# Performance work log

Measured on AMD Instinct MI355X. Metric: run time of the kernel, lower is better.

Reference implementation:

```python
import jax, jax.numpy as jnp
import numpy as np
import math

B, L, H = 32, 2048, 8
DMET, SDIM = 16, 27
DM, NL, DS, TE = 256, 4, 64, 256
LT = L + H - 1
DT_MIN, DT_MAX = 1e-3, 0.1


def setup_inputs() -> dict:
    key = jax.random.key(0)
    ks = jax.random.split(key, 24)
    inp = {
        'x_past': jax.random.normal(ks[0], (B, L, DMET), jnp.float32),
        'noisy_future': jax.random.normal(ks[1], (B, H, 1), jnp.float32),
        't': jax.random.uniform(ks[2], (B,), jnp.float32),
        'x_future': jax.random.normal(ks[3], (B, H - 1, DMET), jnp.float32),
        'static_attr': jax.random.normal(ks[4], (B, 1, SDIM), jnp.float32),
        # MPFourier buffers
        'freqs': 2 * math.pi * jax.random.normal(ks[5], (TE,), jnp.float32),
        'phases': 2 * math.pi * jax.random.uniform(ks[6], (TE,), jnp.float32),
        # input projection (d_met+1+static_dim -> d_model)
        'in_W': jax.random.normal(ks[7], (DMET + 1 + SDIM, DM), jnp.float32) / np.sqrt(DMET + 1 + SDIM),
        'in_b': jnp.zeros((DM,), jnp.float32),
        # time MLP
        'tm_W1': jax.random.normal(ks[8], (TE, 2 * TE), jnp.float32) / np.sqrt(TE),
        'tm_b1': jnp.zeros((2 * TE,), jnp.float32),
        'tm_W2': jax.random.normal(ks[9], (2 * TE, DM), jnp.float32) / np.sqrt(2 * TE),
        'tm_b2': jnp.zeros((DM,), jnp.float32),
        # stacked S4D (LTI) block params, leading dim = n_layers
        'log_dt': jax.random.uniform(ks[10], (NL, DM), jnp.float32) * (math.log(DT_MAX) - math.log(DT_MIN)) + math.log(DT_MIN),
        'A_re': -0.5 * jnp.ones((NL, DM, DS), jnp.float32),
        'A_im': math.pi * jnp.broadcast_to(jnp.arange(DS, dtype=jnp.float32), (NL, DM, DS)),
        'C_re': jax.random.normal(ks[11], (NL, DM, DS), jnp.float32) * (0.5 ** 0.5),
        'C_im': jax.random.normal(ks[12], (NL, DM, DS), jnp.float32) * (0.5 ** 0.5),
        'D': jax.random.normal(ks[13], (NL, DM), jnp.float32),
        'out_W': jax.random.normal(ks[14], (NL, DM, 2 * DM), jnp.float32) / np.sqrt(DM),
        'out_b': jnp.zeros((NL, 2 * DM), jnp.float32),
        # batchnorm
        'bn_gamma': jnp.ones((NL, DM), jnp.float32),
        'bn_beta': jnp.zeros((NL, DM), jnp.float32),
        # head
        'head_W1': jax.random.normal(ks[15], (DM, DM // 2), jnp.float32) / np.sqrt(DM),
        'head_b1': jnp.zeros((DM // 2,), jnp.float32),
        'head_W2': jax.random.normal(ks[16], (DM // 2, 1), jnp.float32) / np.sqrt(DM // 2),
        'head_b2': jnp.zeros((1,), jnp.float32),
    }
    return inp


def _ssm_block(u, log_dt, A_re, A_im, C_re, C_im, D, out_W, out_b):
    # u: [B, d, Lc]. S4D-style diagonal SSM via FFT causal convolution.
    Lc = u.shape[-1]
    dt = jnp.exp(log_dt)                                 # [d]
    A = A_re + 1j * A_im                                 # [d, n], Re(A) < 0
    dtA = dt[:, None] * A                                # [d, n]
    Ck = (C_re + 1j * C_im) * jnp.expm1(dtA) / A         # ZOH-style discretized C
    van = jnp.exp(dtA[:, :, None] * jnp.arange(Lc))      # [d, n, Lc] Vandermonde
    K = 2.0 * jnp.einsum('dn,dnl->dl', Ck, van).real     # [d, Lc]
    nfft = 2 * Lc
    y = jnp.fft.irfft(jnp.fft.rfft(u, nfft) * jnp.fft.rfft(K, nfft)[None], nfft)[..., :Lc]
    y = jax.nn.gelu(y + D[None, :, None] * u)
    z = jnp.einsum('bdl,de->bel', y, out_W) + out_b[None, :, None]  # [B, 2d, Lc]
    z1, z2 = jnp.split(z, 2, axis=1)
    return z1 * jax.nn.sigmoid(z2)                       # GLU


def _batchnorm1d(h, gamma, beta):
    # h: [B, d, Lc]; training-mode batch statistics, eps matches torch default.
    mean = h.mean(axis=(0, 2), keepdims=True)
    var = ((h - mean) ** 2).mean(axis=(0, 2), keepdims=True)
    return (h - mean) * jax.lax.rsqrt(var + 1e-5) * gamma[None, :, None] + beta[None, :, None]


def reference(x_past, noisy_future, t, x_future, static_attr,
              freqs, phases, in_W, in_b, tm_W1, tm_b1, tm_W2, tm_b2,
              log_dt, A_re, A_im, C_re, C_im, D, out_W, out_b,
              bn_gamma, bn_beta, head_W1, head_b1, head_W2, head_b2):
    Bc = x_past.shape[0]
    # MPFourier time features
    t_feats = jnp.cos(t[:, None] * freqs[None, :] + phases[None, :]) * math.sqrt(2)
    t_b = jax.nn.silu(t_feats @ tm_W1 + tm_b1) @ tm_W2 + tm_b2     # [B, DM]
    # feature fusion
    all_met = jnp.concatenate([x_past, x_future], axis=1)          # [B, LT, DMET]
    all_flow = jnp.concatenate([jnp.zeros((Bc, L - 1, 1), x_past.dtype), noisy_future], axis=1)
    static_seq = jnp.broadcast_to(static_attr[:, :1, :], (Bc, LT, SDIM))
    feats = jnp.concatenate([all_met, all_flow, static_seq], axis=-1)
    h = feats @ in_W + in_b                                        # [B, LT, DM]
    h = h.at[:, L - 1:, :].add(t_b[:, None, :])                    # time_full conditioning
    h = jnp.transpose(h, (0, 2, 1))                                # [B, DM, LT]
    for i in range(NL):
        z = _ssm_block(h, log_dt[i], A_re[i], A_im[i], C_re[i], C_im[i],
                       D[i], out_W[i], out_b[i])
        h = _batchnorm1d(h + z, bn_gamma[i], bn_beta[i])           # dropout = identity (eval)
    h = jnp.transpose(h, (0, 2, 1))                                # [B, LT, DM]
    out = jax.nn.silu(h @ head_W1 + head_b1) @ head_W2 + head_b2   # [B, LT, 1]
    return out[:, -H:, :]
```

## Files before the change

kernel.cpp:

```cpp
#include <hip/hip_runtime.h>
#include <hip/hip_bf16.h>
#include <math.h>

#define B_   32
#define L_   2048
#define H_   8
#define DMET 16
#define SDIM 27
#define DM   256
#define NL   4
#define DS   64
#define TE   256
#define LT   2055
#define LTR  2176
#define TCH  128
#define NC   17
#define COLS 544
#define NTOT (B_ * LT)

typedef __attribute__((ext_vector_type(8))) short short8;
typedef __attribute__((ext_vector_type(4))) short short4v;
typedef __attribute__((ext_vector_type(4))) float floatx4;

__device__ __forceinline__ float sigmoidf_(float x) {
    float e = __builtin_amdgcn_exp2f(-1.4426950408889634f * x);
    return __builtin_amdgcn_rcpf(1.0f + e);
}

__device__ __forceinline__ float gelu_tanh(float x) {
    float inner = 1.5957691216057308f * fmaf(0.044715f * x * x, x, x);
    return x * sigmoidf_(inner);
}

__device__ __forceinline__ float fexp_(float x) {
    return __builtin_amdgcn_exp2f(1.4426950408889634f * x);
}
__device__ __forceinline__ float fsin_(float ph) {
    float r = ph * 0.15915494309189535f;
    r = r - floorf(r);
    return __builtin_amdgcn_sinf(r);
}
__device__ __forceinline__ float fcos_(float ph) {
    float r = ph * 0.15915494309189535f;
    r = r - floorf(r);
    return __builtin_amdgcn_cosf(r);
}

__device__ __forceinline__ short bfs(float x) {
    __hip_bfloat16 h = __float2bfloat16(x);
    return *(short*)&h;
}

__device__ __forceinline__ float sbf(short s) {
    unsigned u = ((unsigned)(unsigned short)s) << 16;
    return __uint_as_float(u);
}

__device__ __forceinline__ void glds16(const void* g, void* l) {
    __builtin_amdgcn_global_load_lds(
        (const __attribute__((address_space(1))) unsigned*)g,
        (__attribute__((address_space(3))) unsigned*)l, 16, 0, 0);
}

#define BARV(n) do {                                                          \
    asm volatile("s_waitcnt vmcnt(" #n ") lgkmcnt(0)" ::: "memory");          \
    __builtin_amdgcn_s_barrier();                                             \
    asm volatile("" ::: "memory");                                            \
} while (0)

__global__ __launch_bounds__(256) void time_mlp_kernel(
    const float* __restrict__ t, const float* __restrict__ freqs,
    const float* __restrict__ phases,
    const float* __restrict__ W1, const float* __restrict__ b1,
    const float* __restrict__ W2, const float* __restrict__ b2,
    float* __restrict__ tb) {
    int b = blockIdx.x;
    int tid = threadIdx.x;
    __shared__ float f[TE];
    __shared__ float hid[2 * TE];
    float tv = t[b];
    f[tid] = cosf(fmaf(tv, freqs[tid], phases[tid])) * 1.4142135623730951f;
    __syncthreads();
    float a0 = b1[tid], a1 = b1[tid + TE];
    for (int k = 0; k < TE; ++k) {
        float fk = f[k];
        a0 = fmaf(fk, W1[k * 2 * TE + tid], a0);
        a1 = fmaf(fk, W1[k * 2 * TE + tid + TE], a1);
    }
    hid[tid]      = a0 * sigmoidf_(a0);
    hid[tid + TE] = a1 * sigmoidf_(a1);
    __syncthreads();
    float acc = b2[tid];
    for (int j = 0; j < 2 * TE; ++j)
        acc = fmaf(hid[j], W2[j * DM + tid], acc);
    tb[b * DM + tid] = acc;
}

__global__ __launch_bounds__(256) void wt_prep_kernel(
    const float* __restrict__ out_W, __hip_bfloat16* __restrict__ Wtp) {
    int bid = blockIdx.x;
    int layer = bid >> 8, k = bid & 255;
    int e = threadIdx.x;
    const float* src = out_W + ((size_t)layer * 256 + k) * 512;
    #pragma unroll
    for (int q = 0; q < 2; ++q) {
        int ee = e + q * 256;
        int P = ee & 255, half = ee >> 8;
        int by = P >> 6, pp = P & 63;
        int g = pp >> 5;
        int tcol = (pp & 31) + half * 32;
        int c = by * 128 + g * 64 + tcol;
        Wtp[((size_t)layer * 512 + c) * 256 + k] = __float2bfloat16(src[ee]);
    }
}

__global__ __launch_bounds__(256) void input_proj_kernel(
    const float* __restrict__ xp, const float* __restrict__ nf,
    const float* __restrict__ xf, const float* __restrict__ sa,
    const float* __restrict__ inW, const float* __restrict__ inb,
    const float* __restrict__ tb, __hip_bfloat16* __restrict__ Ub) {
    int b  = blockIdx.y;
    int l0 = blockIdx.x * 256;
    int tx = threadIdx.x;
    int l  = l0 + tx;

    __shared__ float feats[256][18];
    __shared__ float Ws[17][DM];
    __shared__ float sdot[DM];
    __shared__ float tbs[DM];
    __shared__ float sstat[SDIM];

    if (tx < SDIM) sstat[tx] = sa[b * SDIM + tx];
    for (int k = 0; k < 17; ++k) Ws[k][tx] = inW[k * DM + tx];
    tbs[tx] = tb[b * DM + tx];

    bool valid = (l < LT);
    if (valid) {
        const float* src = (l < L_) ? &xp[((size_t)b * L_ + l) * DMET]
                                    : &xf[((size_t)b * (H_ - 1) + (l - L_)) * DMET];
        #pragma unroll
        for (int k = 0; k < DMET; ++k) feats[tx][k] = src[k];
        feats[tx][16] = (l >= L_ - 1) ? nf[b * H_ + (l - (L_ - 1))] : 0.0f;
    }
    __syncthreads();

    float sd = 0.0f;
    for (int k = 0; k < SDIM; ++k)
        sd = fmaf(sstat[k], inW[(17 + k) * DM + tx], sd);
    sdot[tx] = sd;
    __syncthreads();

    if (l >= LTR) return;
    size_t baseb = ((size_t)b * DM) * LTR + l;
    if (!valid) {
        __hip_bfloat16 z = __float2bfloat16(0.0f);
        for (int d = 0; d < DM; ++d) Ub[baseb + (size_t)d * LTR] = z;
        return;
    }
    bool cond = (l >= L_ - 1);
    for (int d = 0; d < DM; ++d) {
        float acc = inb[d] + sdot[d] + (cond ? tbs[d] : 0.0f);
        #pragma unroll
        for (int k = 0; k < 17; ++k)
            acc = fmaf(feats[tx][k], Ws[k][d], acc);
        Ub[baseb + (size_t)d * LTR] = __float2bfloat16(acc);
    }
}

__global__ __launch_bounds__(256) void prep_kernel(
    const float* __restrict__ log_dt,
    const float* __restrict__ A_re, const float* __restrict__ A_im,
    const float* __restrict__ C_re, const float* __restrict__ C_im,
    const float* __restrict__ Dp,
    const float* __restrict__ gamma, const float* __restrict__ beta,
    float* __restrict__ stats, float* __restrict__ scsh,
    __hip_bfloat16* __restrict__ Abig, __hip_bfloat16* __restrict__ SA,
    float* __restrict__ Rsh, float* __restrict__ T1sh, int layer) {
    int d = blockIdx.x;
    int t = threadIdx.x;
    __shared__ float sAr[64], sAi[64], sCkr[64], sCki[64];
    __shared__ float kap[TCH];
    __shared__ float csum[TCH];
    __shared__ float s_sc, s_sh;

    if (t == 0) {
        float sc, sh;
        if (layer == 0) { sc = 1.0f; sh = 0.0f; }
        else {
            float s = stats[d], q = stats[DM + d];
            float mean = s * (1.0f / NTOT);
            float var  = q * (1.0f / NTOT) - mean * mean;
            sc = rsqrtf(var + 1e-5f) * gamma[(layer - 1) * DM + d];
            sh = beta[(layer - 1) * DM + d] - mean * sc;
        }
        s_sc = sc; s_sh = sh;
        scsh[d] = sc; scsh[DM + d] = sh;
        stats[d] = 0.0f; stats[DM + d] = 0.0f;
    }
    __syncthreads();
    float sc = s_sc, sh = s_sh;

    float dt = expf(log_dt[layer * DM + d]);
    float Dd = Dp[layer * DM + d];
    if (t < 64) {
        size_t ab = ((size_t)layer * DM + d) * DS + t;
        float Ar = A_re[ab], Ai = A_im[ab], Cr = C_re[ab], Ci = C_im[ab];
        float ar = dt * Ar, ai = dt * Ai;
        float e = expf(ar);
        float wre = e * cosf(ai), wim = e * sinf(ai);
        float mr = wre - 1.0f, mi = wim;
        float den = 1.0f / (Ar * Ar + Ai * Ai);
        float qr = (mr * Ar + mi * Ai) * den, qi = (mi * Ar - mr * Ai) * den;
        sCkr[t] = Cr * qr - Ci * qi;
        sCki[t] = Cr * qi + Ci * qr;
        sAr[t] = ar;
        sAi[t] = ai;
        float s2 = sinf(0.5f * ai);
        float dr = fmaf(expm1f(ar), cosf(ai), -2.0f * s2 * s2);
        float di = e * sinf(ai);
        float a128 = 128.0f * ar, b128 = 128.0f * ai;
        float s2b = sinf(0.5f * b128);
        float nr = fmaf(expm1f(a128), cosf(b128), -2.0f * s2b * s2b);
        float ni = expf(a128) * sinf(b128);
        float dd2 = 1.0f / (dr * dr + di * di);
        float gr = (nr * dr + ni * di) * dd2;
        float gi = (ni * dr - nr * di) * dd2;
        Rsh[(size_t)d * 128 + t]      = sh * gr;
        Rsh[(size_t)d * 128 + 64 + t] = sh * gi;
    }
    __syncthreads();

    {
        int delta = t >> 1, half = t & 1;
        float fd = (float)delta;
        float p = 0.0f;
        #pragma unroll 8
        for (int n = half * 32; n < half * 32 + 32; ++n) {
            float er = fexp_(fd * sAr[n]);
            float ph = fd * sAi[n];
            p += er * (sCkr[n] * fcos_(ph) - sCki[n] * fsin_(ph));
        }
        p += __shfl_xor(p, 1);
        if (half == 0) kap[delta] = 2.0f * p + (delta == 0 ? Dd : 0.0f);
    }
    __syncthreads();

    if (t < 128) csum[t] = kap[t];
    __syncthreads();
    for (int off = 1; off < 128; off <<= 1) {
        float v = 0.0f;
        if (t >= off && t < 128) v = csum[t - off];
        __syncthreads();
        if (t < 128) csum[t] += v;
        __syncthreads();
    }
    if (t < 128) T1sh[(size_t)d * 128 + t] = sh * csum[t];

    __hip_bfloat16* Ad = Abig + (size_t)d * TCH * 256;
    for (int idx = t; idx < TCH * TCH; idx += 256) {
        int i = idx >> 7, m = idx & 127;
        Ad[(size_t)i * 256 + m] = __float2bfloat16(m <= i ? sc * kap[i - m] : 0.0f);
    }
    for (int idx = t; idx < TCH * 64; idx += 256) {
        int i = idx >> 6, n = idx & 63;
        float fp = (float)(i + 1);
        float er = fexp_(fp * sAr[n]);
        float ph = fp * sAi[n];
        float c = fcos_(ph), s = fsin_(ph);
        float vr = er * (sCkr[n] * c - sCki[n] * s);
        float vi = er * (sCkr[n] * s + sCki[n] * c);
        Ad[(size_t)i * 256 + 128 + n] = __float2bfloat16(2.0f * vr);
        Ad[(size_t)i * 256 + 192 + n] = __float2bfloat16(-2.0f * vi);
    }
    __hip_bfloat16* Sd = SA + (size_t)d * TCH * TCH;
    for (int idx = t; idx < 64 * TCH; idx += 256) {
        int n = idx >> 7, m = idx & 127;
        float fp = (float)(127 - m);
        float er = sc * fexp_(fp * sAr[n]);
        float ph = fp * sAi[n];
        Sd[(size_t)n * 128 + m]        = __float2bfloat16(er * fcos_(ph));
        Sd[(size_t)(64 + n) * 128 + m] = __float2bfloat16(er * fsin_(ph));
    }
}

__global__ __launch_bounds__(256) void sgemm_kernel(
    const __hip_bfloat16* __restrict__ Ub, const __hip_bfloat16* __restrict__ SA,
    const float* __restrict__ Rsh, __hip_bfloat16* __restrict__ S) {
    int id = blockIdx.x;
    int xcd = id & 7, j = id >> 3;
    int dj = (j * 21846) >> 16;
    int d = xcd * 32 + dj;
    int g = j - dj * 3;
    int tid = threadIdx.x, wave = tid >> 6, lane = tid & 63;
    int lm = lane & 15, quad = lane >> 4;
    const __hip_bfloat16* SAd = SA + (size_t)d * TCH * TCH;

    __shared__ short Bs[12288];

    short8 a0r[4], a1r[4];
    #pragma unroll
    for (int kk = 0; kk < 4; ++kk) {
        a0r[kk] = *(const short8*)(SAd + (size_t)(wave * 32 + lm) * TCH + kk * 32 + quad * 8);
        a1r[kk] = *(const short8*)(SAd + (size_t)(wave * 32 + 16 + lm) * TCH + kk * 32 + quad * 8);
    }

    int ntS = (tid >> 6) & 3, qS = (tid >> 4) & 3, ccS = tid & 15;
    const __hip_bfloat16* srcB[3];
    #pragma unroll
    for (int t = 0; t < 3; ++t) {
        int col = (3 * g + t) * 64 + ntS * 16 + ccS;
        int colc = col < COLS ? col : COLS - 1;
        int bh = (colc * 241) >> 12;
        int c = colc - bh * 17;
        srcB[t] = Ub + ((size_t)bh * DM + d) * LTR + (size_t)c * TCH + qS * 8;
    }

    float4 rs0 = *(const float4*)(Rsh + (size_t)d * 128 + wave * 32 + quad * 4);
    float4 rs1 = *(const float4*)(Rsh + (size_t)d * 128 + wave * 32 + 16 + quad * 4);

    floatx4 acc[2][4];
    floatx4 zf = {0.f, 0.f, 0.f, 0.f};
    #pragma unroll
    for (int mi = 0; mi < 2; ++mi)
        #pragma unroll
        for (int nt = 0; nt < 4; ++nt) acc[mi][nt] = zf;

#define SG_STAGE(t_, kk0_, off_)                                              \
    {                                                                         \
        glds16(srcB[t_] + (kk0_) * 32,     (char*)Bs + (off_) + tid * 16);    \
        glds16(srcB[t_] + (kk0_ + 1) * 32, (char*)Bs + (off_) + 4096 + tid * 16); \
    }
#define SG_COMP(off_, kkA_)                                                   \
    {                                                                         \
        const short* bb_ = (const short*)((const char*)Bs + (off_));          \
        _Pragma("unroll")                                                     \
        for (int kk_ = 0; kk_ < 2; ++kk_) {                                   \
            _Pragma("unroll")                                                 \
            for (int nt_ = 0; nt_ < 4; ++nt_) {                               \
                short8 bv = *(const short8*)(bb_ + kk_ * 2048 + nt_ * 512 + lane * 8); \
                acc[0][nt_] = __builtin_amdgcn_mfma_f32_16x16x32_bf16(        \
                    a0r[(kkA_) + kk_], bv, acc[0][nt_], 0, 0, 0);             \
                acc[1][nt_] = __builtin_amdgcn_mfma_f32_16x16x32_bf16(        \
                    a1r[(kkA_) + kk_], bv, acc[1][nt_], 0, 0, 0);             \
            }                                                                 \
        }                                                                     \
    }
#define SG_EPI(cb_)                                                           \
    _Pragma("unroll")                                                         \
    for (int mi = 0; mi < 2; ++mi) {                                          \
        int row = wave * 32 + mi * 16 + quad * 4;                             \
        float4 rs = mi ? rs1 : rs0;                                           \
        _Pragma("unroll")                                                     \
        for (int nt_ = 0; nt_ < 4; ++nt_) {                                   \
            int col = (cb_) * 64 + nt_ * 16 + lm;                             \
            if (col < COLS) {                                                 \
                short4v o;                                                    \
                o[0] = bfs(acc[mi][nt_][0] + rs.x);                           \
                o[1] = bfs(acc[mi][nt_][1] + rs.y);                           \
                o[2] = bfs(acc[mi][nt_][2] + rs.z);                           \
                o[3] = bfs(acc[mi][nt_][3] + rs.w);                           \
                *(short4v*)(S + ((size_t)d * COLS + col) * TCH + row) = o;    \
            }                                                                 \
            acc[mi][nt_] = zf;                                                \
        }                                                                     \
    }

    SG_STAGE(0, 0, 0);
    SG_STAGE(0, 2, 8192);
    SG_STAGE(1, 0, 16384);
    BARV(4);
    SG_COMP(0, 0);
    BARV(2);
    SG_STAGE(1, 2, 0);
    SG_COMP(8192, 2);
    BARV(2);
    SG_STAGE(2, 0, 8192);
    SG_EPI(3 * g + 0);
    BARV(4);
    SG_COMP(16384, 0);
    BARV(2);
    SG_STAGE(2, 2, 16384);
    SG_COMP(0, 2);
    SG_EPI(3 * g + 1);
    BARV(2);
    SG_COMP(8192, 0);
    BARV(0);
    SG_COMP(16384, 2);
    SG_EPI(3 * g + 2);

#undef SG_STAGE
#undef SG_COMP
#undef SG_EPI
}

__global__ __launch_bounds__(64) void carry_kernel(
    __hip_bfloat16* __restrict__ SX,
    const float* __restrict__ log_dt,
    const float* __restrict__ A_re, const float* __restrict__ A_im,
    int layer) {
    int d = blockIdx.x, b = blockIdx.y;
    int n = threadIdx.x;
    float dt = expf(log_dt[layer * DM + d]);
    size_t ab = ((size_t)layer * DM + d) * DS + n;
    float Ar = A_re[ab], Ai = A_im[ab];
    float e = expf(dt * Ar);
    float wre = e * cosf(dt * Ai), wim = e * sinf(dt * Ai);
    #pragma unroll
    for (int t = 0; t < 7; ++t) {
        float r = wre * wre - wim * wim;
        wim = 2.0f * wre * wim; wre = r;
    }
    size_t base = ((size_t)d * COLS + (size_t)b * NC) * TCH + n;
    float sre[NC], sim[NC];
    #pragma unroll
    for (int c = 0; c < NC; ++c) {
        sre[c] = __bfloat162float(SX[base + (size_t)c * TCH]);
        sim[c] = __bfloat162float(SX[base + (size_t)c * TCH + 64]);
    }
    float xr = 0.0f, xi = 0.0f;
    #pragma unroll
    for (int c = 0; c < NC; ++c) {
        SX[base + (size_t)c * TCH]      = __float2bfloat16(xr);
        SX[base + (size_t)c * TCH + 64] = __float2bfloat16(xi);
        float nr = wre * xr - wim * xi + sre[c];
        xi = wre * xi + wim * xr + sim[c];
        xr = nr;
    }
}

__global__ __launch_bounds__(256) void mainscan_kernel(
    const __hip_bfloat16* __restrict__ Ub, const __hip_bfloat16* __restrict__ X,
    const __hip_bfloat16* __restrict__ Abig, const float* __restrict__ T1sh,
    __hip_bfloat16* __restrict__ Ybt) {
    int id = blockIdx.x;
    int xcd = id & 7, j = id >> 3;
    int dj = (j * 21846) >> 16;
    int d = xcd * 32 + dj;
    int g = j - dj * 3;
    int tid = threadIdx.x, wave = tid >> 6, lane = tid & 63;
    int lm = lane & 15, quad = lane >> 4;
    const __hip_bfloat16* Ad = Abig + (size_t)d * TCH * 256;

    __shared__ short Bs[24576];

    short8 a0r[8], a1r[8];
    #pragma unroll
    for (int kk = 0; kk < 8; ++kk) {
        a0r[kk] = *(const short8*)(Ad + (size_t)(wave * 32 + lm) * 256 + kk * 32 + quad * 8);
        a1r[kk] = *(const short8*)(Ad + (size_t)(wave * 32 + 16 + lm) * 256 + kk * 32 + quad * 8);
    }

    int ntS = (tid >> 6) & 3, qS = (tid >> 4) & 3, ccS = tid & 15;
    const __hip_bfloat16* srcU[3];
    const __hip_bfloat16* srcX[3];
    #pragma unroll
    for (int t = 0; t < 3; ++t) {
        int col = (3 * g + t) * 64 + ntS * 16 + ccS;
        int colc = col < COLS ? col : COLS - 1;
        int bh = (colc * 241) >> 12;
        int c = colc - bh * 17;
        srcU[t] = Ub + ((size_t)bh * DM + d) * LTR + (size_t)c * TCH + qS * 8;
        srcX[t] = X + ((size_t)d * COLS + colc) * TCH + qS * 8;
    }

    float4 t1a = *(const float4*)(T1sh + (size_t)d * 128 + wave * 32 + quad * 4);
    float4 t1b = *(const float4*)(T1sh + (size_t)d * 128 + wave * 32 + 16 + quad * 4);

    floatx4 acc[2][4];
    floatx4 zf = {0.f, 0.f, 0.f, 0.f};
    #pragma unroll
    for (int mi = 0; mi < 2; ++mi)
        #pragma unroll
        for (int nt = 0; nt < 4; ++nt) acc[mi][nt] = zf;

#define MS_STAGE_LO(t_, off_)                                                 \
    {                                                                         \
        _Pragma("unroll")                                                     \
        for (int k_ = 0; k_ < 4; ++k_)                                        \
            glds16(srcU[t_] + k_ * 32,                                        \
                   (char*)Bs + (off_) + k_ * 4096 + tid * 16);                \
    }
#define MS_STAGE_HI(t_, off_)                                                 \
    {                                                                         \
        _Pragma("unroll")                                                     \
        for (int k_ = 0; k_ < 4; ++k_)                                        \
            glds16(srcX[t_] + k_ * 32,                                        \
                   (char*)Bs + (off_) + k_ * 4096 + tid * 16);                \
    }
#define MS_COMP(off_, kkA_)                                                   \
    {                                                                         \
        const short* bb_ = (const short*)((const char*)Bs + (off_));          \
        _Pragma("unroll")                                                     \
        for (int kk_ = 0; kk_ < 4; ++kk_) {                                   \
            _Pragma("unroll")                                                 \
            for (int nt_ = 0; nt_ < 4; ++nt_) {                               \
                short8 bv = *(const short8*)(bb_ + kk_ * 2048 + nt_ * 512 + lane * 8); \
                acc[0][nt_] = __builtin_amdgcn_mfma_f32_16x16x32_bf16(        \
                    a0r[(kkA_) + kk_], bv, acc[0][nt_], 0, 0, 0);             \
                acc[1][nt_] = __builtin_amdgcn_mfma_f32_16x16x32_bf16(        \
                    a1r[(kkA_) + kk_], bv, acc[1][nt_], 0, 0, 0);             \
            }                                                                 \
        }                                                                     \
    }
#define MS_EPI(cb_)                                                           \
    _Pragma("unroll")                                                         \
    for (int mi = 0; mi < 2; ++mi) {                                          \
        int row0 = wave * 32 + mi * 16 + quad * 4;                            \
        float4 t1 = mi ? t1b : t1a;                                           \
        _Pragma("unroll")                                                     \
        for (int nt_ = 0; nt_ < 4; ++nt_) {                                   \
            int col = (cb_) * 64 + nt_ * 16 + lm;                             \
            if (col < COLS) {                                                 \
                int bh = (col * 241) >> 12;                                   \
                int c = col - bh * 17;                                        \
                int l0 = c * TCH + row0;                                      \
                float g0 = gelu_tanh(acc[mi][nt_][0] + t1.x);                 \
                float g1 = gelu_tanh(acc[mi][nt_][1] + t1.y);                 \
                float g2 = gelu_tanh(acc[mi][nt_][2] + t1.z);                 \
                float g3 = gelu_tanh(acc[mi][nt_][3] + t1.w);                 \
                __hip_bfloat16* dst = Ybt + ((size_t)bh * DM + d) * LTR + l0; \
                if (l0 + 3 < LT) {                                            \
                    short4v o;                                                \
                    o[0] = bfs(g0); o[1] = bfs(g1);                           \
                    o[2] = bfs(g2); o[3] = bfs(g3);                           \
                    *(short4v*)dst = o;                                       \
                } else {                                                      \
                    if (l0 + 0 < LT) dst[0] = __float2bfloat16(g0);           \
                    if (l0 + 1 < LT) dst[1] = __float2bfloat16(g1);           \
                    if (l0 + 2 < LT) dst[2] = __float2bfloat16(g2);           \
                    if (l0 + 3 < LT) dst[3] = __float2bfloat16(g3);           \
                }                                                             \
            }                                                                 \
            acc[mi][nt_] = zf;                                                \
        }                                                                     \
    }

    MS_STAGE_LO(0, 0);
    MS_STAGE_HI(0, 16384);
    MS_STAGE_LO(1, 32768);
    BARV(8);
    MS_COMP(0, 0);
    BARV(4);
    MS_STAGE_HI(1, 0);
    MS_COMP(16384, 4);
    BARV(4);
    MS_STAGE_LO(2, 16384);
    MS_EPI(3 * g + 0);
    BARV(8);
    MS_COMP(32768, 0);
    BARV(4);
    MS_STAGE_HI(2, 32768);
    MS_COMP(0, 4);
    MS_EPI(3 * g + 1);
    BARV(4);
    MS_COMP(16384, 0);
    BARV(0);
    MS_COMP(32768, 4);
    MS_EPI(3 * g + 2);

#undef MS_STAGE_LO
#undef MS_STAGE_HI
#undef MS_COMP
#undef MS_EPI
}

__global__ __launch_bounds__(256) void gemm_glu_mfma_kernel(
    const __hip_bfloat16* __restrict__ Ybt, __hip_bfloat16* __restrict__ Ub,
    const __hip_bfloat16* __restrict__ Wtp, const float* __restrict__ out_b,
    const float* __restrict__ scsh, float* __restrict__ stats, int layer) {
    int id = blockIdx.x;
    int r8 = id & 7, j = id >> 3;
    int by = r8 >> 1;
    int sub = (r8 & 1) * 272 + j;
    int bq = (sub * 3856) >> 16;
    int bx = sub - bq * 17;
    int b = bq;
    int tid = threadIdx.x;
    int wave = tid >> 6, lane = tid & 63;
    int lm = lane & 15, quad = lane >> 4;
    int l0 = bx * 128;

    __shared__ short lds[16384];

    const __hip_bfloat16* Wl = Wtp + (size_t)layer * 512 * 256 + (size_t)by * 128 * 256;

    int kp = tid >> 4;
    int l8 = tid & 15;
    const __hip_bfloat16* srcA = Ybt + ((size_t)b * DM + 2 * kp) * LTR + l0 + l8 * 8;
    int woff[8];
    {
        int qA = kp >> 2;
        #pragma unroll
        for (int jj = 0; jj < 8; ++jj) {
            int lloc = l8 * 8 + jj;
            int s4 = (qA + lloc + l8) & 3;
            woff[jj] = lloc * 32 + s4 * 8 + (kp & 3) * 2;
        }
    }
    int rB_[2], qB_[2];
    #pragma unroll
    for (int i = 0; i < 2; ++i) {
        int u = i * 256 + tid;
        int r = u >> 2;
        rB_[i] = r;
        qB_[i] = ((u & 3) - r - (r >> 3)) & 3;
    }
    int aoff[4], boff[4];
    #pragma unroll
    for (int mi = 0; mi < 4; ++mi) {
        int r = (wave >> 1) * 64 + mi * 16 + lm;
        aoff[mi] = r * 32 + ((quad + r + (r >> 3)) & 3) * 8;
    }
    #pragma unroll
    for (int ni = 0; ni < 4; ++ni) {
        int r = (wave & 1) * 64 + ni * 16 + lm;
        boff[ni] = r * 32 + ((quad + r + (r >> 3)) & 3) * 8;
    }

    floatx4 acc[4][4];
    floatx4 zf = {0.f, 0.f, 0.f, 0.f};
    #pragma unroll
    for (int mi = 0; mi < 4; ++mi)
        #pragma unroll
        for (int ni = 0; ni < 4; ++ni) acc[mi][ni] = zf;

#define STAGE_B(S, P)                                                         \
    {                                                                         \
        char* bb_ = (char*)(lds + (P) * 8192 + 4096);                         \
        _Pragma("unroll")                                                     \
        for (int i_ = 0; i_ < 2; ++i_)                                        \
            glds16(Wl + (size_t)rB_[i_] * 256 + (S) * 32 + qB_[i_] * 8,       \
                   bb_ + (i_ * 256 + tid) * 16);                              \
    }
#define LOAD_A(S, G0, G1)                                                     \
    {                                                                         \
        const __hip_bfloat16* pa_ = srcA + (size_t)(S) * 32 * LTR;            \
        G0 = *(const short8*)pa_;                                             \
        G1 = *(const short8*)(pa_ + LTR);                                     \
    }
#define WRITE_A(P, G0, G1)                                                    \
    {                                                                         \
        short* ab_ = lds + (P) * 8192;                                        \
        _Pragma("unroll")                                                     \
        for (int j_ = 0; j_ < 8; ++j_) {                                      \
            unsigned pk_ = (unsigned)(unsigned short)G0[j_] |                 \
                           ((unsigned)(unsigned short)G1[j_] << 16);          \
            *(unsigned*)(ab_ + woff[j_]) = pk_;                               \
        }                                                                     \
    }
#define COMPUTE(P)                                                            \
    {                                                                         \
        const short* ab_ = lds + (P) * 8192;                                  \
        const short* bb_ = ab_ + 4096;                                        \
        short8 af_[4], bf_[4];                                                \
        _Pragma("unroll")                                                     \
        for (int mi_ = 0; mi_ < 4; ++mi_)                                     \
            af_[mi_] = *(const short8*)(ab_ + aoff[mi_]);                     \
        _Pragma("unroll")                                                     \
        for (int ni_ = 0; ni_ < 4; ++ni_)                                     \
            bf_[ni_] = *(const short8*)(bb_ + boff[ni_]);                     \
        _Pragma("unroll")                                                     \
        for (int mi_ = 0; mi_ < 4; ++mi_)                                     \
            _Pragma("unroll")                                                 \
            for (int ni_ = 0; ni_ < 4; ++ni_)                                 \
                acc[mi_][ni_] = __builtin_amdgcn_mfma_f32_16x16x32_bf16(      \
                    af_[mi_], bf_[ni_], acc[mi_][ni_], 0, 0, 0);              \
    }
#define FENCE2                                                                \
    asm volatile("s_waitcnt vmcnt(2)" ::: "memory");                          \
    asm volatile("s_waitcnt lgkmcnt(0)" ::: "memory");                        \
    __builtin_amdgcn_sched_barrier(0);                                        \
    __builtin_amdgcn_s_barrier();
#define FENCE0                                                                \
    asm volatile("s_waitcnt vmcnt(0)" ::: "memory");                          \
    asm volatile("s_waitcnt lgkmcnt(0)" ::: "memory");                        \
    __builtin_amdgcn_sched_barrier(0);                                        \
    __builtin_amdgcn_s_barrier();

    short8 gE0, gE1, gO0, gO1;
    STAGE_B(0, 0);
    LOAD_A(0, gE0, gE1);
    WRITE_A(0, gE0, gE1);
    LOAD_A(1, gO0, gO1);
    asm volatile("s_waitcnt lgkmcnt(0)" ::: "memory");
    __builtin_amdgcn_sched_barrier(0);
    __builtin_amdgcn_s_barrier();

    STAGE_B(1, 1); COMPUTE(0); WRITE_A(1, gO0, gO1); LOAD_A(2, gE0, gE1); FENCE2;
    STAGE_B(2, 0); COMPUTE(1); WRITE_A(0, gE0, gE1); LOAD_A(3, gO0, gO1); FENCE2;
    STAGE_B(3, 1); COMPUTE(0); WRITE_A(1, gO0, gO1); LOAD_A(4, gE0, gE1); FENCE2;
    STAGE_B(4, 0); COMPUTE(1); WRITE_A(0, gE0, gE1); LOAD_A(5, gO0, gO1); FENCE2;
    STAGE_B(5, 1); COMPUTE(0); WRITE_A(1, gO0, gO1); LOAD_A(6, gE0, gE1); FENCE2;
    STAGE_B(6, 0); COMPUTE(1); WRITE_A(0, gE0, gE1); LOAD_A(7, gO0, gO1); FENCE2;
    STAGE_B(7, 1); COMPUTE(0); WRITE_A(1, gO0, gO1); FENCE0;
    COMPUTE(1);

#undef STAGE_B
#undef LOAD_A
#undef WRITE_A
#undef COMPUTE
#undef FENCE2
#undef FENCE0

    const float* bl = out_b + layer * 512;
    int Pbase = by * 64 + (wave & 1) * 32;
    int lw = l0 + (wave >> 1) * 64;
    #pragma unroll
    for (int ni = 0; ni < 2; ++ni) {
        int P = Pbase + ni * 16 + lm;
        float bz1 = bl[P], bz2 = bl[256 + P];
        float scP = scsh[P], shP = scsh[DM + P];
        __hip_bfloat16* ubrow = Ub + ((size_t)b * DM + P) * LTR;
        float sp = 0.f, sq = 0.f;
        #pragma unroll
        for (int mi = 0; mi < 4; ++mi) {
            int l0q = lw + mi * 16 + quad * 4;
            if (l0q >= LT) continue;
            floatx4 z1 = acc[mi][ni];
            floatx4 z2 = acc[mi][ni + 2];
            if (l0q + 4 <= LT) {
                short4v uv = *(const short4v*)(ubrow + l0q);
                float h0 = fmaf(scP, sbf(uv[0]), shP) + (z1[0] + bz1) * sigmoidf_(z2[0] + bz2);
                float h1 = fmaf(scP, sbf(uv[1]), shP) + (z1[1] + bz1) * sigmoidf_(z2[1] + bz2);
                float h2 = fmaf(scP, sbf(uv[2]), shP) + (z1[2] + bz1) * sigmoidf_(z2[2] + bz2);
                float h3 = fmaf(scP, sbf(uv[3]), shP) + (z1[3] + bz1) * sigmoidf_(z2[3] + bz2);
                short4v ov;
                ov[0] = bfs(h0); ov[1] = bfs(h1); ov[2] = bfs(h2); ov[3] = bfs(h3);
                *(short4v*)(ubrow + l0q) = ov;
                sp += (h0 + h1) + (h2 + h3);
                sq += (h0 * h0 + h1 * h1) + (h2 * h2 + h3 * h3);
            } else {
                #pragma unroll
                for (int r = 0; r < 4; ++r) {
                    int l = l0q + r;
                    if (l < LT) {
                        float uvv = __bfloat162float(ubrow[l]);
                        float hh = fmaf(scP, uvv, shP) + (z1[r] + bz1) * sigmoidf_(z2[r] + bz2);
                        ubrow[l] = __float2bfloat16(hh);
                        sp += hh; sq += hh * hh;
                    }
                }
            }
        }
        sp += __shfl_xor(sp, 16); sp += __shfl_xor(sp, 32);
        sq += __shfl_xor(sq, 16); sq += __shfl_xor(sq, 32);
        if (quad == 0) {
            atomicAdd(&stats[P], sp);
            atomicAdd(&stats[DM + P], sq);
        }
    }
}

__global__ __launch_bounds__(256) void statsfin_kernel(
    const float* __restrict__ stats,
    const float* __restrict__ gamma, const float* __restrict__ beta,
    float* __restrict__ scsh, int layer) {
    int d = threadIdx.x;
    float s = stats[d], q = stats[DM + d];
    float mean = s * (1.0f / NTOT);
    float var  = q * (1.0f / NTOT) - mean * mean;
    float sc = rsqrtf(var + 1e-5f) * gamma[layer * DM + d];
    scsh[d] = sc;
    scsh[DM + d] = beta[layer * DM + d] - mean * sc;
}

__global__ __launch_bounds__(128) void head_kernel(
    const __hip_bfloat16* __restrict__ Ub, const float* __restrict__ scsh,
    const float* __restrict__ W1, const float* __restrict__ b1,
    const float* __restrict__ W2, const float* __restrict__ b2,
    float* __restrict__ out) {
    int hh = blockIdx.x;
    int b  = blockIdx.y;
    int j  = threadIdx.x;
    int l  = (L_ - 1) + hh;
    const __hip_bfloat16* urow = Ub + ((size_t)b * DM) * LTR + l;
    float a = b1[j];
    for (int k = 0; k < DM; ++k) {
        float hn = fmaf(scsh[k], __bfloat162float(urow[(size_t)k * LTR]), scsh[DM + k]);
        a = fmaf(hn, W1[k * 128 + j], a);
    }
    float hs = a * sigmoidf_(a);
    float v = hs * W2[j];
    v += __shfl_xor(v, 1);
    v += __shfl_xor(v, 2);
    v += __shfl_xor(v, 4);
    v += __shfl_xor(v, 8);
    v += __shfl_xor(v, 16);
    v += __shfl_xor(v, 32);
    __shared__ float partial[2];
    if ((j & 63) == 0) partial[j >> 6] = v;
    __syncthreads();
    if (j == 0) out[b * H_ + hh] = partial[0] + partial[1] + b2[0];
}

extern "C" void kernel_launch(void* const* d_in, const int* in_sizes, int n_in,
                              void* d_out, int out_size, void* d_ws, size_t ws_size,
                              hipStream_t stream) {
    (void)in_sizes; (void)n_in; (void)out_size; (void)ws_size;
    const float* x_past      = (const float*)d_in[0];
    const float* noisy       = (const float*)d_in[1];
    const float* t_in        = (const float*)d_in[2];
    const float* x_future    = (const float*)d_in[3];
    const float* static_attr = (const float*)d_in[4];
    const float* freqs       = (const float*)d_in[5];
    const float* phases      = (const float*)d_in[6];
    const float* in_W        = (const float*)d_in[7];
    const float* in_b        = (const float*)d_in[8];
    const float* tm_W1       = (const float*)d_in[9];
    const float* tm_b1       = (const float*)d_in[10];
    const float* tm_W2       = (const float*)d_in[11];
    const float* tm_b2       = (const float*)d_in[12];
    const float* log_dt      = (const float*)d_in[13];
    const float* A_re        = (const float*)d_in[14];
    const float* A_im        = (const float*)d_in[15];
    const float* C_re        = (const float*)d_in[16];
    const float* C_im        = (const float*)d_in[17];
    const float* Dp          = (const float*)d_in[18];
    const float* out_W       = (const float*)d_in[19];
    const float* out_b       = (const float*)d_in[20];
    const float* bn_gamma    = (const float*)d_in[21];
    const float* bn_beta     = (const float*)d_in[22];
    const float* head_W1     = (const float*)d_in[23];
    const float* head_b1     = (const float*)d_in[24];
    const float* head_W2     = (const float*)d_in[25];
    const float* head_b2     = (const float*)d_in[26];

    char* ws = (char*)d_ws;
    const size_t UB_OFF = 1u << 20;
    const size_t UB_BYT = (size_t)B_ * DM * LTR * 2;
    const size_t R1_OFF = UB_OFF + UB_BYT;
    const size_t RB     = (size_t)256 * COLS * TCH * 2;
    const size_t R2_OFF = R1_OFF + RB;
    const size_t AB_OFF = R2_OFF + RB;
    const size_t AB_BYT = (size_t)256 * TCH * 256 * 2;
    const size_t SA_OFF = AB_OFF + AB_BYT;
    const size_t SA_BYT = (size_t)256 * TCH * TCH * 2;
    const size_t WT_OFF = SA_OFF + SA_BYT;

    float*          tb    = (float*)(ws);
    float*          stats = (float*)(ws + (64 << 10));
    float*          scsh  = (float*)(ws + (96 << 10));
    float*          Rsh   = (float*)(ws + (128 << 10));
    float*          T1sh  = (float*)(ws + (256 << 10));
    __hip_bfloat16* Ub    = (__hip_bfloat16*)(ws + UB_OFF);
    __hip_bfloat16* R1    = (__hip_bfloat16*)(ws + R1_OFF);
    __hip_bfloat16* Ybt   = (__hip_bfloat16*)(ws + R2_OFF);
    __hip_bfloat16* Abig  = (__hip_bfloat16*)(ws + AB_OFF);
    __hip_bfloat16* SA    = (__hip_bfloat16*)(ws + SA_OFF);
    __hip_bfloat16* Wtp   = (__hip_bfloat16*)(ws + WT_OFF);

    time_mlp_kernel<<<dim3(B_), 256, 0, stream>>>(
        t_in, freqs, phases, tm_W1, tm_b1, tm_W2, tm_b2, tb);

    wt_prep_kernel<<<dim3(NL * 256), 256, 0, stream>>>(out_W, Wtp);

    input_proj_kernel<<<dim3(9, B_), 256, 0, stream>>>(
        x_past, noisy, x_future, static_attr, in_W, in_b, tb, Ub);

    for (int layer = 0; layer < NL; ++layer) {
        prep_kernel<<<dim3(256), 256, 0, stream>>>(
            log_dt, A_re, A_im, C_re, C_im, Dp, bn_gamma, bn_beta,
            stats, scsh, Abig, SA, Rsh, T1sh, layer);
        sgemm_kernel<<<dim3(768), 256, 0, stream>>>(Ub, SA, Rsh, R1);
        carry_kernel<<<dim3(256, B_), 64, 0, stream>>>(
            R1, log_dt, A_re, A_im, layer);
        mainscan_kernel<<<dim3(768), 256, 0, stream>>>(Ub, R1, Abig, T1sh, Ybt);
        gemm_glu_mfma_kernel<<<dim3(2176), 256, 0, stream>>>(
            Ybt, Ub, Wtp, out_b, scsh, stats, layer);
    }

    statsfin_kernel<<<dim3(1), 256, 0, stream>>>(
        stats, bn_gamma, bn_beta, scsh, NL - 1);

    head_kernel<<<dim3(H_, B_), 128, 0, stream>>>(
        Ub, scsh, head_W1, head_b1, head_W2, head_b2, (float*)d_out);
}
```

Measured before the change: 703.5 us.

## Keep full A tile resident in LDS and loop over all output column blocks

The GLU GEMM kernel now launches one block per (batch, 128-column L tile) instead of four. It loads the whole 256-deep A slice into LDS once, then iterates over the four 128-wide weight column groups, streaming B tiles and running the fused GLU/residual/stats epilogue after each group. This removes the fourfold re-read of Ybt from global memory. In exchange, LDS use per block rises from 32 KB to 80 KB and the grid shrinks to 544 blocks, which lowers occupancy and parallelism and serialises four epilogues within each block.

```diff
diff --git a/kernel.cpp b/kernel.cpp
--- a/kernel.cpp
+++ b/kernel.cpp
@@ -568,10 +568,7 @@
     const __hip_bfloat16* __restrict__ Ybt, __hip_bfloat16* __restrict__ Ub,
     const __hip_bfloat16* __restrict__ Wtp, const float* __restrict__ out_b,
     const float* __restrict__ scsh, float* __restrict__ stats, int layer) {
-    int id = blockIdx.x;
-    int r8 = id & 7, j = id >> 3;
-    int by = r8 >> 1;
-    int sub = (r8 & 1) * 272 + j;
+    int sub = blockIdx.x;
     int bq = (sub * 3856) >> 16;
     int bx = sub - bq * 17;
     int b = bq;
@@ -580,21 +577,19 @@
     int lm = lane & 15, quad = lane >> 4;
     int l0 = bx * 128;
 
-    __shared__ short lds[16384];
-
-    const __hip_bfloat16* Wl = Wtp + (size_t)layer * 512 * 256 + (size_t)by * 128 * 256;
+    __shared__ short lds[40960];
 
     int kp = tid >> 4;
     int l8 = tid & 15;
     const __hip_bfloat16* srcA = Ybt + ((size_t)b * DM + 2 * kp) * LTR + l0 + l8 * 8;
-    int woff[8];
+    int pbA[8], lbA[8];
     {
-        int qA = kp >> 2;
+        int kg4 = kp >> 2;
         #pragma unroll
         for (int jj = 0; jj < 8; ++jj) {
             int lloc = l8 * 8 + jj;
-            int s4 = (qA + lloc + l8) & 3;
-            woff[jj] = lloc * 32 + s4 * 8 + (kp & 3) * 2;
+            pbA[jj] = kg4 + lloc + (lloc >> 3);
+            lbA[jj] = lloc * 256 + (kp & 3) * 2;
         }
     }
     int rB_[2], qB_[2];
@@ -605,12 +600,14 @@
         rB_[i] = r;
         qB_[i] = ((u & 3) - r - (r >> 3)) & 3;
     }
-    int aoff[4], boff[4];
+    int rA_[4], abA_[4];
     #pragma unroll
     for (int mi = 0; mi < 4; ++mi) {
         int r = (wave >> 1) * 64 + mi * 16 + lm;
-        aoff[mi] = r * 32 + ((quad + r + (r >> 3)) & 3) * 8;
-    }
+        rA_[mi] = r * 256;
+        abA_[mi] = quad + r + (r >> 3);
+    }
+    int boff[4];
     #pragma unroll
     for (int ni = 0; ni < 4; ++ni) {
         int r = (wave & 1) * 64 + ni * 16 + lm;
@@ -624,12 +621,15 @@
         #pragma unroll
         for (int ni = 0; ni < 4; ++ni) acc[mi][ni] = zf;
 
-#define STAGE_B(S, P)                                                         \
+    const float* bl = out_b + layer * 512;
+    int lwq = l0 + (wave >> 1) * 64;
+
+#define STAGE_B(S, P, WB)                                                     \
     {                                                                         \
-        char* bb_ = (char*)(lds + (P) * 8192 + 4096);                         \
+        char* bb_ = (char*)(lds + 32768 + (P) * 4096);                        \
         _Pragma("unroll")                                                     \
         for (int i_ = 0; i_ < 2; ++i_)                                        \
-            glds16(Wl + (size_t)rB_[i_] * 256 + (S) * 32 + qB_[i_] * 8,       \
+            glds16((WB) + (size_t)rB_[i_] * 256 + (S) * 32 + qB_[i_] * 8,     \
                    bb_ + (i_ * 256 + tid) * 16);                              \
     }
 #define LOAD_A(S, G0, G1)                                                     \
@@ -638,24 +638,24 @@
         G0 = *(const short8*)pa_;                                             \
         G1 = *(const short8*)(pa_ + LTR);                                     \
     }
-#define WRITE_A(P, G0, G1)                                                    \
+#define WRITE_A(S, G0, G1)                                                    \
     {                                                                         \
-        short* ab_ = lds + (P) * 8192;                                        \
         _Pragma("unroll")                                                     \
         for (int j_ = 0; j_ < 8; ++j_) {                                      \
             unsigned pk_ = (unsigned)(unsigned short)G0[j_] |                 \
                            ((unsigned)(unsigned short)G1[j_] << 16);          \
-            *(unsigned*)(ab_ + woff[j_]) = pk_;                               \
+            int off_ = lbA[j_] + (((S) * 4 + pbA[j_]) & 31) * 8;              \
+            *(unsigned*)(lds + off_) = pk_;                                   \
         }                                                                     \
     }
-#define COMPUTE(P)                                                            \
+#define COMPUTE(S, P)                                                         \
     {                                                                         \
-        const short* ab_ = lds + (P) * 8192;                                  \
-        const short* bb_ = ab_ + 4096;                                        \
+        const short* bb_ = lds + 32768 + (P) * 4096;                          \
         short8 af_[4], bf_[4];                                                \
         _Pragma("unroll")                                                     \
         for (int mi_ = 0; mi_ < 4; ++mi_)                                     \
-            af_[mi_] = *(const short8*)(ab_ + aoff[mi_]);                     \
+            af_[mi_] = *(const short8*)(lds + rA_[mi_] +                      \
+                         (((S) * 4 + abA_[mi_]) & 31) * 8);                   \
         _Pragma("unroll")                                                     \
         for (int ni_ = 0; ni_ < 4; ++ni_)                                     \
             bf_[ni_] = *(const short8*)(bb_ + boff[ni_]);                     \
@@ -666,89 +666,115 @@
                 acc[mi_][ni_] = __builtin_amdgcn_mfma_f32_16x16x32_bf16(      \
                     af_[mi_], bf_[ni_], acc[mi_][ni_], 0, 0, 0);              \
     }
+#define EPILOGUE(BY)                                                          \
+    {                                                                         \
+        int Pbase_ = (BY) * 64 + (wave & 1) * 32;                             \
+        _Pragma("unroll")                                                     \
+        for (int ni = 0; ni < 2; ++ni) {                                      \
+            int P = Pbase_ + ni * 16 + lm;                                    \
+            float bz1 = bl[P], bz2 = bl[256 + P];                             \
+            float scP = scsh[P], shP = scsh[DM + P];                          \
+            __hip_bfloat16* ubrow = Ub + ((size_t)b * DM + P) * LTR;          \
+            float sp = 0.f, sq = 0.f;                                         \
+            _Pragma("unroll")                                                 \
+            for (int mi = 0; mi < 4; ++mi) {                                  \
+                int l0q = lwq + mi * 16 + quad * 4;                           \
+                floatx4 z1 = acc[mi][ni];                                     \
+                floatx4 z2 = acc[mi][ni + 2];                                 \
+                acc[mi][ni] = zf; acc[mi][ni + 2] = zf;                       \
+                if (l0q >= LT) continue;                                      \
+                if (l0q + 4 <= LT) {                                          \
+                    short4v uv = *(const short4v*)(ubrow + l0q);              \
+                    float h0 = fmaf(scP, sbf(uv[0]), shP) +                   \
+                               (z1[0] + bz1) * sigmoidf_(z2[0] + bz2);        \
+                    float h1 = fmaf(scP, sbf(uv[1]), shP) +                   \
+                               (z1[1] + bz1) * sigmoidf_(z2[1] + bz2);        \
+                    float h2 = fmaf(scP, sbf(uv[2]), shP) +                   \
+                               (z1[2] + bz1) * sigmoidf_(z2[2] + bz2);        \
+                    float h3 = fmaf(scP, sbf(uv[3]), shP) +                   \
+                               (z1[3] + bz1) * sigmoidf_(z2[3] + bz2);        \
+                    short4v ov;                                               \
+                    ov[0] = bfs(h0); ov[1] = bfs(h1);                         \
+                    ov[2] = bfs(h2); ov[3] = bfs(h3);                         \
+                    *(short4v*)(ubrow + l0q) = ov;                            \
+                    sp += (h0 + h1) + (h2 + h3);                              \
+                    sq += (h0 * h0 + h1 * h1) + (h2 * h2 + h3 * h3);          \
+                } else {                                                      \
+                    _Pragma("unroll")                                         \
+                    for (int r = 0; r < 4; ++r) {                             \
+                        int l = l0q + r;                                      \
+                        if (l < LT) {                                         \
+                            float uvv = __bfloat162float(ubrow[l]);           \
+                            float hh = fmaf(scP, uvv, shP) +                  \
+                                (z1[r] + bz1) * sigmoidf_(z2[r] + bz2);       \
+                            ubrow[l] = __float2bfloat16(hh);                  \
+                            sp += hh; sq += hh * hh;                          \
+                        }                                                     \
+                    }                                                         \
+                }                                                             \
+            }                                                                 \
+            sp += __shfl_xor(sp, 16); sp += __shfl_xor(sp, 32);               \
+            sq += __shfl_xor(sq, 16); sq += __shfl_xor(sq, 32);               \
+            if (quad == 0) {                                                  \
+                atomicAdd(&stats[P], sp);                                     \
+                atomicAdd(&stats[DM + P], sq);                                \
+            }                                                                 \
+        }                                                                     \
+    }
 #define FENCE2                                                                \
-    asm volatile("s_waitcnt vmcnt(2)" ::: "memory");                          \
-    asm volatile("s_waitcnt lgkmcnt(0)" ::: "memory");                        \
+    asm volatile("s_waitcnt vmcnt(2) lgkmcnt(0)" ::: "memory");               \
     __builtin_amdgcn_sched_barrier(0);                                        \
     __builtin_amdgcn_s_barrier();
 #define FENCE0                                                                \
-    asm volatile("s_waitcnt vmcnt(0)" ::: "memory");                          \
-    asm volatile("s_waitcnt lgkmcnt(0)" ::: "memory");                        \
+    asm volatile("s_waitcnt vmcnt(0) lgkmcnt(0)" ::: "memory");               \
     __builtin_amdgcn_sched_barrier(0);                                        \
     __builtin_amdgcn_s_barrier();
 
+    const __hip_bfloat16* Wl = Wtp + (size_t)layer * 512 * 256;
+
     short8 gE0, gE1, gO0, gO1;
-    STAGE_B(0, 0);
+    STAGE_B(0, 0, Wl);
     LOAD_A(0, gE0, gE1);
     WRITE_A(0, gE0, gE1);
     LOAD_A(1, gO0, gO1);
-    asm volatile("s_waitcnt lgkmcnt(0)" ::: "memory");
-    __builtin_amdgcn_sched_barrier(0);
-    __builtin_amdgcn_s_barrier();
-
-    STAGE_B(1, 1); COMPUTE(0); WRITE_A(1, gO0, gO1); LOAD_A(2, gE0, gE1); FENCE2;
-    STAGE_B(2, 0); COMPUTE(1); WRITE_A(0, gE0, gE1); LOAD_A(3, gO0, gO1); FENCE2;
-    STAGE_B(3, 1); COMPUTE(0); WRITE_A(1, gO0, gO1); LOAD_A(4, gE0, gE1); FENCE2;
-    STAGE_B(4, 0); COMPUTE(1); WRITE_A(0, gE0, gE1); LOAD_A(5, gO0, gO1); FENCE2;
-    STAGE_B(5, 1); COMPUTE(0); WRITE_A(1, gO0, gO1); LOAD_A(6, gE0, gE1); FENCE2;
-    STAGE_B(6, 0); COMPUTE(1); WRITE_A(0, gE0, gE1); LOAD_A(7, gO0, gO1); FENCE2;
-    STAGE_B(7, 1); COMPUTE(0); WRITE_A(1, gO0, gO1); FENCE0;
-    COMPUTE(1);
+    FENCE2;
+
+    STAGE_B(1, 1, Wl); COMPUTE(0, 0); WRITE_A(1, gO0, gO1); LOAD_A(2, gE0, gE1); FENCE2;
+    STAGE_B(2, 0, Wl); COMPUTE(1, 1); WRITE_A(2, gE0, gE1); LOAD_A(3, gO0, gO1); FENCE2;
+    STAGE_B(3, 1, Wl); COMPUTE(2, 0); WRITE_A(3, gO0, gO1); LOAD_A(4, gE0, gE1); FENCE2;
+    STAGE_B(4, 0, Wl); COMPUTE(3, 1); WRITE_A(4, gE0, gE1); LOAD_A(5, gO0, gO1); FENCE2;
+    STAGE_B(5, 1, Wl); COMPUTE(4, 0); WRITE_A(5, gO0, gO1); LOAD_A(6, gE0, gE1); FENCE2;
+    STAGE_B(6, 0, Wl); COMPUTE(5, 1); WRITE_A(6, gE0, gE1); LOAD_A(7, gO0, gO1); FENCE2;
+    STAGE_B(7, 1, Wl); COMPUTE(6, 0); WRITE_A(7, gO0, gO1); FENCE0;
+    STAGE_B(0, 0, Wl + 32768);
+    COMPUTE(7, 1);
+    EPILOGUE(0);
+    BARV(0);
+
+    const __hip_bfloat16* Wn = Wl + 32768;
+    for (int by = 1; by < 4; ++by) {
+        #pragma unroll
+        for (int s = 0; s < 7; ++s) {
+            STAGE_B(s + 1, (s + 1) & 1, Wn);
+            COMPUTE(s, s & 1);
+            BARV(0);
+        }
+        if (by < 3) STAGE_B(0, 0, Wn + 32768);
+        COMPUTE(7, 1);
+        EPILOGUE(by);
+        if (by < 3) {
+            BARV(0);
+            Wn += 32768;
+        }
+    }
 
 #undef STAGE_B
 #undef LOAD_A
 #undef WRITE_A
 #undef COMPUTE
+#undef EPILOGUE
 #undef FENCE2
 #undef FENCE0
-
-    const float* bl = out_b + layer * 512;
-    int Pbase = by * 64 + (wave & 1) * 32;
-    int lw = l0 + (wave >> 1) * 64;
-    #pragma unroll
-    for (int ni = 0; ni < 2; ++ni) {
-        int P = Pbase + ni * 16 + lm;
-        float bz1 = bl[P], bz2 = bl[256 + P];
-        float scP = scsh[P], shP = scsh[DM + P];
-        __hip_bfloat16* ubrow = Ub + ((size_t)b * DM + P) * LTR;
-        float sp = 0.f, sq = 0.f;
-        #pragma unroll
-        for (int mi = 0; mi < 4; ++mi) {
-            int l0q = lw + mi * 16 + quad * 4;
-            if (l0q >= LT) continue;
-            floatx4 z1 = acc[mi][ni];
-            floatx4 z2 = acc[mi][ni + 2];
-            if (l0q + 4 <= LT) {
-                short4v uv = *(const short4v*)(ubrow + l0q);
-                float h0 = fmaf(scP, sbf(uv[0]), shP) + (z1[0] + bz1) * sigmoidf_(z2[0] + bz2);
-                float h1 = fmaf(scP, sbf(uv[1]), shP) + (z1[1] + bz1) * sigmoidf_(z2[1] + bz2);
-                float h2 = fmaf(scP, sbf(uv[2]), shP) + (z1[2] + bz1) * sigmoidf_(z2[2] + bz2);
-                float h3 = fmaf(scP, sbf(uv[3]), shP) + (z1[3] + bz1) * sigmoidf_(z2[3] + bz2);
-                short4v ov;
-                ov[0] = bfs(h0); ov[1] = bfs(h1); ov[2] = bfs(h2); ov[3] = bfs(h3);
-                *(short4v*)(ubrow + l0q) = ov;
-                sp += (h0 + h1) + (h2 + h3);
-                sq += (h0 * h0 + h1 * h1) + (h2 * h2 + h3 * h3);
-            } else {
-                #pragma unroll
-                for (int r = 0; r < 4; ++r) {
-                    int l = l0q + r;
-                    if (l < LT) {
-                        float uvv = __bfloat162float(ubrow[l]);
-                        float hh = fmaf(scP, uvv, shP) + (z1[r] + bz1) * sigmoidf_(z2[r] + bz2);
-                        ubrow[l] = __float2bfloat16(hh);
-                        sp += hh; sq += hh * hh;
-                    }
-                }
-            }
-        }
-        sp += __shfl_xor(sp, 16); sp += __shfl_xor(sp, 32);
-        sq += __shfl_xor(sq, 16); sq += __shfl_xor(sq, 32);
-        if (quad == 0) {
-            atomicAdd(&stats[P], sp);
-            atomicAdd(&stats[DM + P], sq);
-        }
-    }
 }
 
 __global__ __launch_bounds__(256) void statsfin_kernel(
@@ -865,7 +891,7 @@
         carry_kernel<<<dim3(256, B_), 64, 0, stream>>>(
             R1, log_dt, A_re, A_im, layer);
         mainscan_kernel<<<dim3(768), 256, 0, stream>>>(Ub, R1, Abig, T1sh, Ybt);
-        gemm_glu_mfma_kernel<<<dim3(2176), 256, 0, stream>>>(
+        gemm_glu_mfma_kernel<<<dim3(544), 256, 0, stream>>>(
             Ybt, Ub, Wtp, out_b, scsh, stats, layer);
     }
 
```

After: 874.5 us. 1.24x slower.
